# Kernel tuning notes

Measured on AMD Instinct MI355X. Metric: run time of the kernel, lower is better.

The kernel has to match this reference:

```python
import jax, jax.numpy as jnp
import numpy as np

B, S, C, H, D = 4, 2048, 512, 8, 64
EPS = 1e-5
SCALE = D ** -0.5


def layer_norm(x, w, b):
    m = jnp.mean(x, axis=-1, keepdims=True)
    v = jnp.var(x, axis=-1, keepdims=True)
    return (x - m) * jax.lax.rsqrt(v + EPS) * w + b


def setup_inputs() -> dict:
    key = jax.random.key(0)
    ks = jax.random.split(key, 7)
    s = 0.02
    return {
        "x": jax.random.normal(ks[0], (B, S, C), jnp.float32),
        "Wq": jax.random.normal(ks[1], (C, H * D), jnp.float32) * s,
        "Wk": jax.random.normal(ks[2], (C, H * D), jnp.float32) * s,
        "Wv": jax.random.normal(ks[3], (C, H * D), jnp.float32) * s,
        "Wo": jax.random.normal(ks[4], (H * D, C), jnp.float32) * s,
        "ln1_w": jnp.ones((C,), jnp.float32), "ln1_b": jnp.zeros((C,), jnp.float32),
        "ff_ln1_w": jnp.ones((C,), jnp.float32), "ff_ln1_b": jnp.zeros((C,), jnp.float32),
        "ff_w1": jax.random.normal(ks[5], (C, C), jnp.float32) * s, "ff_b1": jnp.zeros((C,), jnp.float32),
        "ff_ln2_w": jnp.ones((C,), jnp.float32), "ff_ln2_b": jnp.zeros((C,), jnp.float32),
        "ff_w2": jax.random.normal(ks[6], (C, C), jnp.float32) * s, "ff_b2": jnp.zeros((C,), jnp.float32),
        "ln2_w": jnp.ones((C,), jnp.float32), "ln2_b": jnp.zeros((C,), jnp.float32),
    }


def causal_attention(x, Wq, Wk, Wv, Wo):
    # Mathematically identical to the bucketed memory-efficient attention:
    # online-softmax bucketing changes compute order, not the result.
    q = (x @ Wq).reshape(B, S, H, D).transpose(0, 2, 1, 3)  # [B,H,S,D]
    k = (x @ Wk).reshape(B, S, H, D).transpose(0, 2, 1, 3)
    v = (x @ Wv).reshape(B, S, H, D).transpose(0, 2, 1, 3)
    scores = jnp.einsum('bhqd,bhkd->bhqk', q, k) * SCALE  # [B,H,S,S]
    causal = jnp.tril(jnp.ones((S, S), bool))
    scores = jnp.where(causal, scores, jnp.finfo(scores.dtype).min)
    attn = jax.nn.softmax(scores, axis=-1)
    out = jnp.einsum('bhqk,bhkd->bhqd', attn, v)
    out = out.transpose(0, 2, 1, 3).reshape(B, S, H * D)
    return out @ Wo


def reference(x, Wq, Wk, Wv, Wo, ln1_w, ln1_b, ff_ln1_w, ff_ln1_b, ff_w1, ff_b1,
              ff_ln2_w, ff_ln2_b, ff_w2, ff_b2, ln2_w, ln2_b):
    a = causal_attention(x, Wq, Wk, Wv, Wo)
    x_ln = layer_norm(a + x, ln1_w, ln1_b)
    h = layer_norm(x_ln, ff_ln1_w, ff_ln1_b) @ ff_w1 + ff_b1
    h = layer_norm(h, ff_ln2_w, ff_ln2_b) @ ff_w2 + ff_b2
    return layer_norm(h + x_ln, ln2_w, ln2_b)
```

## Files before the change

### kernel.cpp

```cpp
#include <hip/hip_runtime.h>

#define B_ 4
#define S_ 2048
#define C_ 512
#define H_ 8
#define D_ 64
#define M_ 8192

typedef short s8v __attribute__((ext_vector_type(8)));
typedef short s4v __attribute__((ext_vector_type(4)));
typedef float f4v __attribute__((ext_vector_type(4)));
typedef unsigned short u16;
typedef unsigned int u32;

__device__ __forceinline__ u16 f2b(float f) {
    u32 u = __builtin_bit_cast(u32, f);
    u = u + 0x7fffu + ((u >> 16) & 1u);
    return (u16)(u >> 16);
}

__device__ __forceinline__ void b2f8(const s8v v, float* f) {
    #pragma unroll
    for (int k = 0; k < 8; ++k)
        f[k] = __builtin_bit_cast(float, (u32)(u16)v[k] << 16);
}

__device__ __forceinline__ void gl2lds16(const void* g, void* l) {
    __builtin_amdgcn_global_load_lds(
        (const __attribute__((address_space(1))) void*)g,
        (__attribute__((address_space(3))) void*)l, 16, 0, 0);
}

__global__ __launch_bounds__(256) void prep_k(const float* __restrict__ x,
                                              u16* __restrict__ xb,
                                              const float* __restrict__ s0,
                                              const float* __restrict__ s1,
                                              const float* __restrict__ s2,
                                              const float* __restrict__ s3,
                                              const float* __restrict__ s4,
                                              const float* __restrict__ s5,
                                              u16* __restrict__ d0,
                                              u16* __restrict__ d1,
                                              u16* __restrict__ d2,
                                              u16* __restrict__ d3,
                                              u16* __restrict__ d4,
                                              u16* __restrict__ d5)
{
    __shared__ float t[32][33];
    const int bx = blockIdx.x;
    if (bx < 4096) {
        const int i = (bx * 256 + (int)threadIdx.x) * 4;
        const float4 v = *(const float4*)&x[i];
        ushort4 o;
        o.x = f2b(v.x); o.y = f2b(v.y); o.z = f2b(v.z); o.w = f2b(v.w);
        *(ushort4*)&xb[i] = o;
        return;
    }
    const int tb = bx - 4096;
    const int z = tb >> 8, rem = tb & 255;
    const float* W; u16* Wt;
    switch (z) {
        case 0: W = s0; Wt = d0; break;
        case 1: W = s1; Wt = d1; break;
        case 2: W = s2; Wt = d2; break;
        case 3: W = s3; Wt = d3; break;
        case 4: W = s4; Wt = d4; break;
        default: W = s5; Wt = d5; break;
    }
    const int tx = threadIdx.x & 31, ty = threadIdx.x >> 5;
    const int n0 = (rem & 15) * 32, k0 = (rem >> 4) * 32;
    #pragma unroll
    for (int i = 0; i < 4; ++i)
        t[ty + i * 8][tx] = W[(size_t)(k0 + ty + i * 8) * C_ + n0 + tx];
    __syncthreads();
    #pragma unroll
    for (int i = 0; i < 4; ++i)
        Wt[(size_t)(n0 + ty + i * 8) * C_ + k0 + tx] = f2b(t[tx][ty + i * 8]);
}

template <bool OB>
__global__ __launch_bounds__(256) void gemm_k(const u16* __restrict__ A,
                                              const u16* __restrict__ Bt,
                                              const float* __restrict__ bias,
                                              void* __restrict__ outv)
{
    __shared__ u16 As[2][128][64];
    __shared__ u16 Bs[2][64][64];
    const int tid = threadIdx.x;
    const int lane = tid & 63, w = tid >> 6;
    const int q4 = lane >> 4, l16 = lane & 15;
    const int wr = w >> 1, wc = w & 1;
    const int bm = blockIdx.x * 128, bn = blockIdx.y * 64;
    const int sr8  = lane >> 3;
    const int scol = ((lane & 7) ^ sr8) * 8;

    f4v acc[4][2];
    #pragma unroll
    for (int i = 0; i < 4; ++i)
        #pragma unroll
        for (int j = 0; j < 2; ++j) acc[i][j] = (f4v){0.f, 0.f, 0.f, 0.f};

    const u16* Ab = A  + (size_t)bm * C_;
    const u16* Bb = Bt + (size_t)bn * C_;

    auto stage = [&](int bf, int kt) {
        const int k0 = kt * 64;
        #pragma unroll
        for (int t = 0; t < 4; ++t)
            gl2lds16(Ab + (size_t)(w * 32 + t * 8 + sr8) * C_ + k0 + scol,
                     (char*)As + bf * 16384 + (w * 32 + t * 8) * 128);
        #pragma unroll
        for (int t = 0; t < 2; ++t)
            gl2lds16(Bb + (size_t)(w * 16 + t * 8 + sr8) * C_ + k0 + scol,
                     (char*)Bs + bf * 8192 + (w * 16 + t * 8) * 128);
    };

    stage(0, 0);
    for (int kt = 0; kt < 8; ++kt) {
        __syncthreads();
        const int bf = kt & 1;
        if (kt < 7) stage(bf ^ 1, kt + 1);
        #pragma unroll
        for (int kk = 0; kk < 2; ++kk) {
            const int pc = ((kk * 4 + q4) ^ (l16 & 7)) * 8;
            s8v a[4], b[2];
            #pragma unroll
            for (int i = 0; i < 4; ++i)
                a[i] = *(const s8v*)&As[bf][wr * 64 + i * 16 + l16][pc];
            #pragma unroll
            for (int j = 0; j < 2; ++j)
                b[j] = *(const s8v*)&Bs[bf][wc * 32 + j * 16 + l16][pc];
            #pragma unroll
            for (int i = 0; i < 4; ++i)
                #pragma unroll
                for (int j = 0; j < 2; ++j)
                    acc[i][j] = __builtin_amdgcn_mfma_f32_16x16x32_bf16(a[i], b[j], acc[i][j], 0, 0, 0);
        }
    }

    if constexpr (OB) {
        __syncthreads();
        u16* Ls = (u16*)As;
        #pragma unroll
        for (int j = 0; j < 2; ++j) {
            const int nl = wc * 32 + j * 16 + l16;
            const float bj = bias ? bias[bn + nl] : 0.0f;
            #pragma unroll
            for (int i = 0; i < 4; ++i) {
                const int ml = wr * 64 + i * 16 + q4 * 4;
                #pragma unroll
                for (int reg = 0; reg < 4; ++reg)
                    Ls[(ml + reg) * 72 + nl] = f2b(acc[i][j][reg] + bj);
            }
        }
        __syncthreads();
        #pragma unroll
        for (int pass = 0; pass < 4; ++pass) {
            const int idx = tid + pass * 256;
            const int r = idx >> 3, c = idx & 7;
            const s8v v = *(const s8v*)&Ls[r * 72 + c * 8];
            *(s8v*)&((u16*)outv)[(size_t)(bm + r) * C_ + bn + c * 8] = v;
        }
    } else {
        #pragma unroll
        for (int j = 0; j < 2; ++j) {
            const int n = bn + wc * 32 + j * 16 + l16;
            const float bj = bias ? bias[n] : 0.0f;
            #pragma unroll
            for (int i = 0; i < 4; ++i) {
                const int m = bm + wr * 64 + i * 16 + q4 * 4;
                #pragma unroll
                for (int reg = 0; reg < 4; ++reg)
                    ((float*)outv)[(size_t)(m + reg) * C_ + n] = acc[i][j][reg] + bj;
            }
        }
    }
}

__global__ __launch_bounds__(256) void qkv_k(const u16* __restrict__ A,
                                             const u16* __restrict__ Wq,
                                             const u16* __restrict__ Wk,
                                             const u16* __restrict__ Wv,
                                             u16* __restrict__ oq,
                                             u16* __restrict__ ok,
                                             u16* __restrict__ ovt)
{
    __shared__ u16 As[2][128][64];
    __shared__ u16 Bs[2][64][64];
    const int tid = threadIdx.x;
    const int lane = tid & 63, w = tid >> 6;
    const int q4 = lane >> 4, l16 = lane & 15;
    const int wr = w >> 1, wc = w & 1;
    const int nt = blockIdx.y, which = nt >> 3;
    const u16* Bt = which == 0 ? Wq : (which == 1 ? Wk : Wv);
    const int bm = blockIdx.x * 128, bn = (nt & 7) * 64;
    const int sr8  = lane >> 3;
    const int scol = ((lane & 7) ^ sr8) * 8;

    f4v acc[4][2];
    #pragma unroll
    for (int i = 0; i < 4; ++i)
        #pragma unroll
        for (int j = 0; j < 2; ++j) acc[i][j] = (f4v){0.f, 0.f, 0.f, 0.f};

    const u16* Ab = A  + (size_t)bm * C_;
    const u16* Bb = Bt + (size_t)bn * C_;

    auto stage = [&](int bf, int kt) {
        const int k0 = kt * 64;
        #pragma unroll
        for (int t = 0; t < 4; ++t)
            gl2lds16(Ab + (size_t)(w * 32 + t * 8 + sr8) * C_ + k0 + scol,
                     (char*)As + bf * 16384 + (w * 32 + t * 8) * 128);
        #pragma unroll
        for (int t = 0; t < 2; ++t)
            gl2lds16(Bb + (size_t)(w * 16 + t * 8 + sr8) * C_ + k0 + scol,
                     (char*)Bs + bf * 8192 + (w * 16 + t * 8) * 128);
    };

    stage(0, 0);
    for (int kt = 0; kt < 8; ++kt) {
        __syncthreads();
        const int bf = kt & 1;
        if (kt < 7) stage(bf ^ 1, kt + 1);
        #pragma unroll
        for (int kk = 0; kk < 2; ++kk) {
            const int pc = ((kk * 4 + q4) ^ (l16 & 7)) * 8;
            s8v a[4], b[2];
            #pragma unroll
            for (int i = 0; i < 4; ++i)
                a[i] = *(const s8v*)&As[bf][wr * 64 + i * 16 + l16][pc];
            #pragma unroll
            for (int j = 0; j < 2; ++j)
                b[j] = *(const s8v*)&Bs[bf][wc * 32 + j * 16 + l16][pc];
            #pragma unroll
            for (int i = 0; i < 4; ++i)
                #pragma unroll
                for (int j = 0; j < 2; ++j)
                    acc[i][j] = __builtin_amdgcn_mfma_f32_16x16x32_bf16(a[i], b[j], acc[i][j], 0, 0, 0);
        }
    }

    if (which < 2) {
        __syncthreads();
        u16* Ls = (u16*)As;
        #pragma unroll
        for (int j = 0; j < 2; ++j) {
            const int nl = wc * 32 + j * 16 + l16;
            #pragma unroll
            for (int i = 0; i < 4; ++i) {
                const int ml = wr * 64 + i * 16 + q4 * 4;
                #pragma unroll
                for (int reg = 0; reg < 4; ++reg)
                    Ls[(ml + reg) * 72 + nl] = f2b(acc[i][j][reg]);
            }
        }
        __syncthreads();
        u16* dst = which == 0 ? oq : ok;
        #pragma unroll
        for (int pass = 0; pass < 4; ++pass) {
            const int idx = tid + pass * 256;
            const int r = idx >> 3, c = idx & 7;
            const s8v v = *(const s8v*)&Ls[r * 72 + c * 8];
            const int cg = which == 0 ? c : ((c & ~3) | ((c & 3) ^ ((r >> 2) & 3)));
            *(s8v*)&dst[(size_t)(bm + r) * C_ + bn + cg * 8] = v;
        }
    } else {
        const int bglob = bm >> 11;
        const int sbase = bm & (S_ - 1);
        #pragma unroll
        for (int j = 0; j < 2; ++j) {
            const int n = bn + wc * 32 + j * 16 + l16;
            const int h = n >> 6, d = n & 63;
            u16* vrow = ovt + ((size_t)(bglob * H_ + h) * D_ + d) * S_;
            const int xw = d & 7;
            #pragma unroll
            for (int i = 0; i < 4; ++i) {
                const int s = sbase + wr * 64 + i * 16 + q4 * 4;
                const int pg = ((s & 31) >> 2) ^ xw;
                s4v pv;
                #pragma unroll
                for (int reg = 0; reg < 4; ++reg) pv[reg] = (short)f2b(acc[i][j][reg]);
                *(s4v*)&vrow[(s & ~31) + (pg << 2)] = pv;
            }
        }
    }
}

__global__ __launch_bounds__(256) void ln2xb_k(const u16* __restrict__ in,
                                               const float* __restrict__ res,
                                               const float* __restrict__ w1,
                                               const float* __restrict__ b1,
                                               const float* __restrict__ w2,
                                               const float* __restrict__ b2,
                                               u16* __restrict__ out1,
                                               u16* __restrict__ out2)
{
    const int lane = threadIdx.x & 63;
    const int row  = blockIdx.x * 4 + (threadIdx.x >> 6);
    const size_t off = (size_t)row * C_ + lane * 8;
    float v[8];
    b2f8(*(const s8v*)&in[off], v);
    {
        const float4 r0 = *(const float4*)&res[off];
        const float4 r1 = *(const float4*)&res[off + 4];
        v[0] += r0.x; v[1] += r0.y; v[2] += r0.z; v[3] += r0.w;
        v[4] += r1.x; v[5] += r1.y; v[6] += r1.z; v[7] += r1.w;
    }
    float s = 0.f, ss = 0.f;
    #pragma unroll
    for (int k = 0; k < 8; ++k) { s += v[k]; ss += v[k] * v[k]; }
    #pragma unroll
    for (int o = 32; o >= 1; o >>= 1) { s += __shfl_xor(s, o); ss += __shfl_xor(ss, o); }
    float mean = s * (1.0f / C_);
    float rstd = rsqrtf(ss * (1.0f / C_) - mean * mean + 1e-5f);

    const float4 wA0 = *(const float4*)&w1[lane * 8];
    const float4 wA1 = *(const float4*)&w1[lane * 8 + 4];
    const float4 bA0 = *(const float4*)&b1[lane * 8];
    const float4 bA1 = *(const float4*)&b1[lane * 8 + 4];
    const float wA[8] = {wA0.x, wA0.y, wA0.z, wA0.w, wA1.x, wA1.y, wA1.z, wA1.w};
    const float bA[8] = {bA0.x, bA0.y, bA0.z, bA0.w, bA1.x, bA1.y, bA1.z, bA1.w};
    float y[8];
    s8v o1;
    #pragma unroll
    for (int k = 0; k < 8; ++k) {
        y[k] = (v[k] - mean) * rstd * wA[k] + bA[k];
        o1[k] = (short)f2b(y[k]);
    }
    *(s8v*)&out1[off] = o1;

    s = 0.f; ss = 0.f;
    #pragma unroll
    for (int k = 0; k < 8; ++k) { s += y[k]; ss += y[k] * y[k]; }
    #pragma unroll
    for (int o = 32; o >= 1; o >>= 1) { s += __shfl_xor(s, o); ss += __shfl_xor(ss, o); }
    mean = s * (1.0f / C_);
    rstd = rsqrtf(ss * (1.0f / C_) - mean * mean + 1e-5f);

    const float4 wB0 = *(const float4*)&w2[lane * 8];
    const float4 wB1 = *(const float4*)&w2[lane * 8 + 4];
    const float4 bB0 = *(const float4*)&b2[lane * 8];
    const float4 bB1 = *(const float4*)&b2[lane * 8 + 4];
    const float wB[8] = {wB0.x, wB0.y, wB0.z, wB0.w, wB1.x, wB1.y, wB1.z, wB1.w};
    const float bB[8] = {bB0.x, bB0.y, bB0.z, bB0.w, bB1.x, bB1.y, bB1.z, bB1.w};
    s8v o2;
    #pragma unroll
    for (int k = 0; k < 8; ++k)
        o2[k] = (short)f2b((y[k] - mean) * rstd * wB[k] + bB[k]);
    *(s8v*)&out2[off] = o2;
}

__global__ __launch_bounds__(256) void lnb_k(const u16* __restrict__ in,
                                             const float* __restrict__ w,
                                             const float* __restrict__ bb,
                                             u16* __restrict__ out)
{
    const int lane = threadIdx.x & 63;
    const int row  = blockIdx.x * 4 + (threadIdx.x >> 6);
    const size_t off = (size_t)row * C_ + lane * 8;
    float v[8];
    b2f8(*(const s8v*)&in[off], v);
    float s = 0.f, ss = 0.f;
    #pragma unroll
    for (int k = 0; k < 8; ++k) { s += v[k]; ss += v[k] * v[k]; }
    #pragma unroll
    for (int o = 32; o >= 1; o >>= 1) { s += __shfl_xor(s, o); ss += __shfl_xor(ss, o); }
    const float mean = s * (1.0f / C_);
    const float rstd = rsqrtf(ss * (1.0f / C_) - mean * mean + 1e-5f);
    const float4 w0 = *(const float4*)&w[lane * 8];
    const float4 w1 = *(const float4*)&w[lane * 8 + 4];
    const float4 b0 = *(const float4*)&bb[lane * 8];
    const float4 b1 = *(const float4*)&bb[lane * 8 + 4];
    const float wv[8] = {w0.x, w0.y, w0.z, w0.w, w1.x, w1.y, w1.z, w1.w};
    const float bv[8] = {b0.x, b0.y, b0.z, b0.w, b1.x, b1.y, b1.z, b1.w};
    s8v o;
    #pragma unroll
    for (int k = 0; k < 8; ++k)
        o[k] = (short)f2b((v[k] - mean) * rstd * wv[k] + bv[k]);
    *(s8v*)&out[off] = o;
}

__global__ __launch_bounds__(256) void lnfin_k(const u16* __restrict__ in,
                                               const u16* __restrict__ res,
                                               const float* __restrict__ w,
                                               const float* __restrict__ bb,
                                               float* __restrict__ out)
{
    const int lane = threadIdx.x & 63;
    const int row  = blockIdx.x * 4 + (threadIdx.x >> 6);
    const size_t off = (size_t)row * C_ + lane * 8;
    float v[8], r[8];
    b2f8(*(const s8v*)&in[off], v);
    b2f8(*(const s8v*)&res[off], r);
    #pragma unroll
    for (int k = 0; k < 8; ++k) v[k] += r[k];
    float s = 0.f, ss = 0.f;
    #pragma unroll
    for (int k = 0; k < 8; ++k) { s += v[k]; ss += v[k] * v[k]; }
    #pragma unroll
    for (int o = 32; o >= 1; o >>= 1) { s += __shfl_xor(s, o); ss += __shfl_xor(ss, o); }
    const float mean = s * (1.0f / C_);
    const float rstd = rsqrtf(ss * (1.0f / C_) - mean * mean + 1e-5f);
    const float4 w0 = *(const float4*)&w[lane * 8];
    const float4 w1 = *(const float4*)&w[lane * 8 + 4];
    const float4 b0 = *(const float4*)&bb[lane * 8];
    const float4 b1 = *(const float4*)&bb[lane * 8 + 4];
    const float wv[8] = {w0.x, w0.y, w0.z, w0.w, w1.x, w1.y, w1.z, w1.w};
    const float bv[8] = {b0.x, b0.y, b0.z, b0.w, b1.x, b1.y, b1.z, b1.w};
    float4 o0, o1;
    o0.x = (v[0] - mean) * rstd * wv[0] + bv[0];
    o0.y = (v[1] - mean) * rstd * wv[1] + bv[1];
    o0.z = (v[2] - mean) * rstd * wv[2] + bv[2];
    o0.w = (v[3] - mean) * rstd * wv[3] + bv[3];
    o1.x = (v[4] - mean) * rstd * wv[4] + bv[4];
    o1.y = (v[5] - mean) * rstd * wv[5] + bv[5];
    o1.z = (v[6] - mean) * rstd * wv[6] + bv[6];
    o1.w = (v[7] - mean) * rstd * wv[7] + bv[7];
    *(float4*)&out[off]     = o0;
    *(float4*)&out[off + 4] = o1;
}

__global__ __launch_bounds__(512, 4) void attn_k(const u16* __restrict__ Q,
                                                 const u16* __restrict__ K,
                                                 const u16* __restrict__ Vt,
                                                 u16* __restrict__ O)
{
    __shared__ char smem[65536];
    u16* KsB = (u16*)smem;
    u16* VsB = (u16*)(smem + 32768);
    const int tid = threadIdx.x;
    const int lane = tid & 63, w = tid >> 6;
    const int grp = w >> 2, wl = w & 3;
    const int q4 = lane >> 4, l16 = lane & 15;
    const int h = blockIdx.x, px = blockIdx.y, b = blockIdx.z;
    const int qH = 31 - px, qL = px;
    const int nH = 32 - px;
    const size_t base  = ((size_t)b * S_) * C_ + h * D_;
    const size_t basev = ((size_t)(b * H_ + h)) * D_ * S_;
    const int lr = lane >> 2, lc = (lane & 3) * 8;
    const int kq = (q4 ^ ((l16 >> 2) & 3)) * 8;
    const int qrow = wl * 16 + l16;

    const u16* ksA = KsB + grp * 4096;
    const u16* ksBp = KsB + (grp + 2) * 4096;
    const u16* vsA = VsB + grp * 4096;
    const u16* vsBp = VsB + (grp + 2) * 4096;
    char* kdA = (char*)KsB + grp * 8192 + wl * 1024;
    char* kdB = (char*)KsB + (grp + 2) * 8192 + wl * 1024;
    char* vdA = (char*)VsB + grp * 8192 + wl * 1024;
    char* vdB = (char*)VsB + (grp + 2) * 8192 + wl * 1024;

    const int kfb = l16 * 32 + kq;
    int vfb[4];
    #pragma unroll
    for (int c = 0; c < 4; ++c)
        vfb[c] = l16 * 32 + ((((c & 1) * 4 + q4) ^ (l16 & 7)) * 4);

    const u16* kpt = K  + base  + (size_t)(wl * 16 + lr) * C_ + lc;
    const u16* vpt = Vt + basev + (size_t)(wl * 16 + lr) * S_ + lc;

    f4v acc[4]; float lp[4];
    f4v oH[4];  float lpH[4];
    #pragma unroll
    for (int j = 0; j < 4; ++j) {
        acc[j] = (f4v){0.f, 0.f, 0.f, 0.f}; lp[j] = 0.f;
        oH[j]  = (f4v){0.f, 0.f, 0.f, 0.f}; lpH[j] = 0.f;
    }
    s8v qf[2];
    #pragma unroll
    for (int kh = 0; kh < 2; ++kh)
        qf[kh] = *(const s8v*)&Q[base + (size_t)(qH * 64 + qrow) * C_ + kh * 32 + q4 * 8];

    bool dumped = false, wrapped = false;

    auto dumpacc = [&]() {
        #pragma unroll
        for (int j = 0; j < 4; ++j) {
            oH[j] = acc[j]; lpH[j] = lp[j];
            acc[j] = (f4v){0.f, 0.f, 0.f, 0.f}; lp[j] = 0.f;
        }
        #pragma unroll
        for (int kh = 0; kh < 2; ++kh)
            qf[kh] = *(const s8v*)&Q[base + (size_t)(qL * 64 + qrow) * C_ + kh * 32 + q4 * 8];
    };

    auto compute = [&](const u16* ks, const u16* vs, const bool diag) {
        f4v sc[4];
        #pragma unroll
        for (int j = 0; j < 4; ++j) sc[j] = (f4v){0.f, 0.f, 0.f, 0.f};
        __builtin_amdgcn_s_setprio(1);
        #pragma unroll
        for (int kh = 0; kh < 2; ++kh)
            #pragma unroll
            for (int j = 0; j < 4; ++j) {
                const s8v kf = *(const s8v*)&ks[kfb + kh * 2048 + j * 512];
                sc[j] = __builtin_amdgcn_mfma_f32_16x16x32_bf16(kf, qf[kh], sc[j], 0, 0, 0);
            }
        __builtin_amdgcn_s_setprio(0);
        s4v pa[4];
        if (diag) {
            #pragma unroll
            for (int j = 0; j < 4; ++j) {
                float ps = 0.0f;
                #pragma unroll
                for (int reg = 0; reg < 4; ++reg) {
                    float tt = fmaf(sc[j][reg], 0.18033688011112043f, -11.541560327111707f);
                    if ((j * 16 + q4 * 4 + reg) > qrow) tt = -128.0f;
                    const float p = exp2f(tt);
                    ps += p;
                    pa[j][reg] = (short)(__builtin_bit_cast(u32, p) >> 16);
                }
                lp[j] += ps;
            }
        } else {
            #pragma unroll
            for (int j = 0; j < 4; ++j) {
                float ps = 0.0f;
                #pragma unroll
                for (int reg = 0; reg < 4; ++reg) {
                    const float p = exp2f(fmaf(sc[j][reg], 0.18033688011112043f,
                                               -11.541560327111707f));
                    ps += p;
                    pa[j][reg] = (short)(__builtin_bit_cast(u32, p) >> 16);
                }
                lp[j] += ps;
            }
        }
        __builtin_amdgcn_s_setprio(1);
        #pragma unroll
        for (int c = 0; c < 4; ++c)
            #pragma unroll
            for (int dj = 0; dj < 4; ++dj) {
                const s4v vb = *(const s4v*)&vs[vfb[c] + (c >> 1) * 2048 + dj * 512];
                acc[dj] = __builtin_amdgcn_mfma_f32_16x16x16bf16_1k(pa[c], vb, acc[dj], 0, 0, 0);
            }
        __builtin_amdgcn_s_setprio(0);
    };

    {
        const u16* kc = kpt + (size_t)(grp * 64) * C_;
        const u16* vc = vpt + grp * 64;
        gl2lds16(kc, kdA); gl2lds16(kc + 32, kdA + 4096);
        gl2lds16(vc, vdA); gl2lds16(vc + 32, vdA + 4096);
    }
    const u16* kcur = kpt + (size_t)((grp + 2) * 64) * C_;
    const u16* vcur = vpt + (grp + 2) * 64;
    int snext = grp + 2;
    int s = grp;

    auto advance = [&]() {
        kcur += (size_t)128 * C_;
        vcur += 128;
        snext += 2;
        if (!wrapped && snext >= nH) {
            kcur -= (size_t)(nH * 64) * C_;
            vcur -= nH * 64;
            wrapped = true;
        }
    };

    for (int u = 0; u < 8; ++u) {
        __syncthreads();
        {
            gl2lds16(kcur, kdB); gl2lds16(kcur + 32, kdB + 4096);
            gl2lds16(vcur, vdB); gl2lds16(vcur + 32, vdB + 4096);
            advance();
        }
        if (!dumped && s >= nH) { dumped = true; dumpacc(); }
        compute(ksA, vsA, (s == nH - 1) || (s == 32));
        s += 2;
        __syncthreads();
        if (u < 7 || grp == 0) {
            gl2lds16(kcur, kdA); gl2lds16(kcur + 32, kdA + 4096);
            gl2lds16(vcur, vdA); gl2lds16(vcur + 32, vdA + 4096);
            advance();
        }
        if (!dumped && s >= nH) { dumped = true; dumpacc(); }
        compute(ksBp, vsBp, (s == nH - 1) || (s == 32));
        s += 2;
    }
    __syncthreads();
    if (grp == 0) {
        if (!dumped) { dumped = true; dumpacc(); }
        compute(ksA, vsA, true);
    }
    if (!dumped) {
        #pragma unroll
        for (int j = 0; j < 4; ++j) {
            oH[j] = acc[j]; lpH[j] = lp[j];
            acc[j] = (f4v){0.f, 0.f, 0.f, 0.f}; lp[j] = 0.f;
        }
    }

    __syncthreads();
    float* exH = (float*)smem;
    float* exL = (float*)(smem + 20480);
    {
        float* p = (grp ? exH : exL) + (wl * 64 + lane) * 20;
        if (grp) {
            #pragma unroll
            for (int dj = 0; dj < 4; ++dj)
                #pragma unroll
                for (int reg = 0; reg < 4; ++reg) p[dj * 4 + reg] = oH[dj][reg];
            #pragma unroll
            for (int j = 0; j < 4; ++j) p[16 + j] = lpH[j];
        } else {
            #pragma unroll
            for (int dj = 0; dj < 4; ++dj)
                #pragma unroll
                for (int reg = 0; reg < 4; ++reg) p[dj * 4 + reg] = acc[dj][reg];
            #pragma unroll
            for (int j = 0; j < 4; ++j) p[16 + j] = lp[j];
        }
    }
    __syncthreads();
    if (grp == 0) {
        const float* p = exH + (wl * 64 + lane) * 20;
        #pragma unroll
        for (int dj = 0; dj < 4; ++dj)
            #pragma unroll
            for (int reg = 0; reg < 4; ++reg) oH[dj][reg] += p[dj * 4 + reg];
        #pragma unroll
        for (int j = 0; j < 4; ++j) lpH[j] += p[16 + j];
        float lt = (lpH[0] + lpH[1]) + (lpH[2] + lpH[3]);
        lt += __shfl_xor(lt, 16);
        lt += __shfl_xor(lt, 32);
        #pragma unroll
        for (int reg = 0; reg < 4; ++reg) {
            const float inv = 1.0f / __shfl(lt, q4 * 4 + reg);
            const size_t rowoff = base + (size_t)(qH * 64 + wl * 16 + q4 * 4 + reg) * C_;
            #pragma unroll
            for (int dj = 0; dj < 4; ++dj)
                O[rowoff + dj * 16 + l16] = f2b(oH[dj][reg] * inv);
        }
    } else {
        const float* p = exL + (wl * 64 + lane) * 20;
        #pragma unroll
        for (int dj = 0; dj < 4; ++dj)
            #pragma unroll
            for (int reg = 0; reg < 4; ++reg) acc[dj][reg] += p[dj * 4 + reg];
        #pragma unroll
        for (int j = 0; j < 4; ++j) lp[j] += p[16 + j];
        float lt = (lp[0] + lp[1]) + (lp[2] + lp[3]);
        lt += __shfl_xor(lt, 16);
        lt += __shfl_xor(lt, 32);
        #pragma unroll
        for (int reg = 0; reg < 4; ++reg) {
            const float inv = 1.0f / __shfl(lt, q4 * 4 + reg);
            const size_t rowoff = base + (size_t)(qL * 64 + wl * 16 + q4 * 4 + reg) * C_;
            #pragma unroll
            for (int dj = 0; dj < 4; ++dj)
                O[rowoff + dj * 16 + l16] = f2b(acc[dj][reg] * inv);
        }
    }
}

extern "C" void kernel_launch(void* const* d_in, const int* in_sizes, int n_in,
                              void* d_out, int out_size, void* d_ws, size_t ws_size,
                              hipStream_t stream)
{
    const float* x       = (const float*)d_in[0];
    const float* Wq      = (const float*)d_in[1];
    const float* Wk      = (const float*)d_in[2];
    const float* Wv      = (const float*)d_in[3];
    const float* Wo      = (const float*)d_in[4];
    const float* ln1_w   = (const float*)d_in[5];
    const float* ln1_b   = (const float*)d_in[6];
    const float* ffln1_w = (const float*)d_in[7];
    const float* ffln1_b = (const float*)d_in[8];
    const float* ff_w1   = (const float*)d_in[9];
    const float* ff_b1   = (const float*)d_in[10];
    const float* ffln2_w = (const float*)d_in[11];
    const float* ffln2_b = (const float*)d_in[12];
    const float* ff_w2   = (const float*)d_in[13];
    const float* ff_b2   = (const float*)d_in[14];
    const float* ln2_w   = (const float*)d_in[15];
    const float* ln2_b   = (const float*)d_in[16];
    float* out = (float*)d_out;

    const size_t MC = (size_t)M_ * C_;
    const size_t WW = (size_t)C_ * C_;
    u16* xb   = (u16*)d_ws;
    u16* WqT  = xb + MC;
    u16* WkT  = WqT + WW;
    u16* WvT  = WkT + WW;
    u16* WoT  = WvT + WW;
    u16* W1T  = WoT + WW;
    u16* W2T  = W1T + WW;
    u16* qbuf = W2T + WW;
    u16* kbuf = qbuf + MC;
    u16* vbuf = kbuf + MC;
    u16* vtbuf= vbuf + MC;
    u16*  abuf = xb;
    u16*  tf   = qbuf;
    u16*  xln  = vbuf;

    const dim3 gg(M_ / 128, C_ / 64);
    const dim3 gq(M_ / 128, 24);
    const dim3 ga(H_, 16, B_);
    const int  gl = M_ / 4;

    prep_k<<<5632, 256, 0, stream>>>(x, xb, Wq, Wk, Wv, Wo, ff_w1, ff_w2,
                                     WqT, WkT, WvT, WoT, W1T, W2T);

    qkv_k<<<gq, 256, 0, stream>>>(xb, WqT, WkT, WvT, qbuf, kbuf, vtbuf);
    attn_k<<<ga, 512, 0, stream>>>(qbuf, kbuf, vtbuf, abuf);

    gemm_k<true><<<gg, 256, 0, stream>>>(abuf, WoT, nullptr, tf);
    ln2xb_k<<<gl, 256, 0, stream>>>(tf, x, ln1_w, ln1_b, ffln1_w, ffln1_b,
                                    xln, xb);
    gemm_k<true><<<gg, 256, 0, stream>>>(xb, W1T, ff_b1, tf);
    lnb_k<<<gl, 256, 0, stream>>>(tf, ffln2_w, ffln2_b, xb);
    gemm_k<true><<<gg, 256, 0, stream>>>(xb, W2T, ff_b2, tf);
    lnfin_k<<<gl, 256, 0, stream>>>(tf, xln, ln2_w, ln2_b, out);
}
```

Measured before the change: 219.7 us.

## Halve attention key tile to 32 and double blocks per CU

The causal attention kernel now streams K/V in 32-key sub-tiles instead of 64-key tiles. That halves the shared-memory staging buffers and each compute step's score and probability registers, and the occupancy hint rises from 4 to 8 blocks. Loop count, wrap logic, diagonal masking (now with a per-subtile offset) and the final tail step are reworked to match. The goal is higher occupancy and better latency hiding, at the cost of twice as many barriers and smaller MFMA batches per sync.

```diff
diff --git a/kernel.cpp b/kernel.cpp
--- a/kernel.cpp
+++ b/kernel.cpp
@@ -421,52 +421,53 @@
     *(float4*)&out[off + 4] = o1;
 }
 
-__global__ __launch_bounds__(512, 4) void attn_k(const u16* __restrict__ Q,
+__global__ __launch_bounds__(512, 8) void attn_k(const u16* __restrict__ Q,
                                                  const u16* __restrict__ K,
                                                  const u16* __restrict__ Vt,
                                                  u16* __restrict__ O)
 {
-    __shared__ char smem[65536];
+    __shared__ char smem[40960];
     u16* KsB = (u16*)smem;
-    u16* VsB = (u16*)(smem + 32768);
+    u16* VsB = (u16*)(smem + 16384);
     const int tid = threadIdx.x;
     const int lane = tid & 63, w = tid >> 6;
     const int grp = w >> 2, wl = w & 3;
     const int q4 = lane >> 4, l16 = lane & 15;
     const int h = blockIdx.x, px = blockIdx.y, b = blockIdx.z;
     const int qH = 31 - px, qL = px;
-    const int nH = 32 - px;
+    const int nHp = 64 - 2 * px;
     const size_t base  = ((size_t)b * S_) * C_ + h * D_;
     const size_t basev = ((size_t)(b * H_ + h)) * D_ * S_;
-    const int lr = lane >> 2, lc = (lane & 3) * 8;
     const int kq = (q4 ^ ((l16 >> 2) & 3)) * 8;
     const int qrow = wl * 16 + l16;
 
-    const u16* ksA = KsB + grp * 4096;
-    const u16* ksBp = KsB + (grp + 2) * 4096;
-    const u16* vsA = VsB + grp * 4096;
-    const u16* vsBp = VsB + (grp + 2) * 4096;
-    char* kdA = (char*)KsB + grp * 8192 + wl * 1024;
-    char* kdB = (char*)KsB + (grp + 2) * 8192 + wl * 1024;
-    char* vdA = (char*)VsB + grp * 8192 + wl * 1024;
-    char* vdB = (char*)VsB + (grp + 2) * 8192 + wl * 1024;
+    const u16* ksA  = KsB + grp * 2048;
+    const u16* ksBp = KsB + (grp + 2) * 2048;
+    const u16* vsA  = VsB + grp * 2048;
+    const u16* vsBp = VsB + (grp + 2) * 2048;
+    char* kdA = (char*)KsB + grp * 4096 + wl * 1024;
+    char* kdB = (char*)KsB + (grp + 2) * 4096 + wl * 1024;
+    char* vdA = (char*)VsB + grp * 4096 + wl * 1024;
+    char* vdB = (char*)VsB + (grp + 2) * 4096 + wl * 1024;
 
     const int kfb = l16 * 32 + kq;
-    int vfb[4];
-    #pragma unroll
-    for (int c = 0; c < 4; ++c)
-        vfb[c] = l16 * 32 + ((((c & 1) * 4 + q4) ^ (l16 & 7)) * 4);
-
-    const u16* kpt = K  + base  + (size_t)(wl * 16 + lr) * C_ + lc;
-    const u16* vpt = Vt + basev + (size_t)(wl * 16 + lr) * S_ + lc;
-
-    f4v acc[4]; float lp[4];
-    f4v oH[4];  float lpH[4];
+    int vfb[2];
+    #pragma unroll
+    for (int c = 0; c < 2; ++c)
+        vfb[c] = l16 * 32 + ((((c * 4 + q4)) ^ (l16 & 7)) * 4);
+
+    const int ldr = wl * 16 + (lane >> 2);
+    const u16* kpt2 = K  + base  + (size_t)(ldr & 31) * C_ + (ldr >> 5) * 32 + (lane & 3) * 8;
+    const u16* vpt2 = Vt + basev + (size_t)ldr * S_ + (lane & 3) * 8;
+
+    f4v acc[4]; float lp[2];
+    f4v oH[4];  float lpH[2];
     #pragma unroll
     for (int j = 0; j < 4; ++j) {
-        acc[j] = (f4v){0.f, 0.f, 0.f, 0.f}; lp[j] = 0.f;
-        oH[j]  = (f4v){0.f, 0.f, 0.f, 0.f}; lpH[j] = 0.f;
-    }
+        acc[j] = (f4v){0.f, 0.f, 0.f, 0.f};
+        oH[j]  = (f4v){0.f, 0.f, 0.f, 0.f};
+    }
+    lp[0] = lp[1] = lpH[0] = lpH[1] = 0.f;
     s8v qf[2];
     #pragma unroll
     for (int kh = 0; kh < 2; ++kh)
@@ -477,36 +478,37 @@
     auto dumpacc = [&]() {
         #pragma unroll
         for (int j = 0; j < 4; ++j) {
-            oH[j] = acc[j]; lpH[j] = lp[j];
-            acc[j] = (f4v){0.f, 0.f, 0.f, 0.f}; lp[j] = 0.f;
-        }
+            oH[j] = acc[j];
+            acc[j] = (f4v){0.f, 0.f, 0.f, 0.f};
+        }
+        lpH[0] = lp[0]; lpH[1] = lp[1]; lp[0] = lp[1] = 0.f;
         #pragma unroll
         for (int kh = 0; kh < 2; ++kh)
             qf[kh] = *(const s8v*)&Q[base + (size_t)(qL * 64 + qrow) * C_ + kh * 32 + q4 * 8];
     };
 
-    auto compute = [&](const u16* ks, const u16* vs, const bool diag) {
-        f4v sc[4];
-        #pragma unroll
-        for (int j = 0; j < 4; ++j) sc[j] = (f4v){0.f, 0.f, 0.f, 0.f};
+    auto compute = [&](const u16* ks, const u16* vs, const int mbase) {
+        f4v sc[2];
+        sc[0] = (f4v){0.f, 0.f, 0.f, 0.f};
+        sc[1] = (f4v){0.f, 0.f, 0.f, 0.f};
         __builtin_amdgcn_s_setprio(1);
         #pragma unroll
         for (int kh = 0; kh < 2; ++kh)
             #pragma unroll
-            for (int j = 0; j < 4; ++j) {
-                const s8v kf = *(const s8v*)&ks[kfb + kh * 2048 + j * 512];
+            for (int j = 0; j < 2; ++j) {
+                const s8v kf = *(const s8v*)&ks[kfb + kh * 1024 + j * 512];
                 sc[j] = __builtin_amdgcn_mfma_f32_16x16x32_bf16(kf, qf[kh], sc[j], 0, 0, 0);
             }
         __builtin_amdgcn_s_setprio(0);
-        s4v pa[4];
-        if (diag) {
-            #pragma unroll
-            for (int j = 0; j < 4; ++j) {
+        s4v pa[2];
+        if (mbase >= 0) {
+            #pragma unroll
+            for (int j = 0; j < 2; ++j) {
                 float ps = 0.0f;
                 #pragma unroll
                 for (int reg = 0; reg < 4; ++reg) {
                     float tt = fmaf(sc[j][reg], 0.18033688011112043f, -11.541560327111707f);
-                    if ((j * 16 + q4 * 4 + reg) > qrow) tt = -128.0f;
+                    if ((mbase + j * 16 + q4 * 4 + reg) > qrow) tt = -128.0f;
                     const float p = exp2f(tt);
                     ps += p;
                     pa[j][reg] = (short)(__builtin_bit_cast(u32, p) >> 16);
@@ -515,7 +517,7 @@
             }
         } else {
             #pragma unroll
-            for (int j = 0; j < 4; ++j) {
+            for (int j = 0; j < 2; ++j) {
                 float ps = 0.0f;
                 #pragma unroll
                 for (int reg = 0; reg < 4; ++reg) {
@@ -529,69 +531,54 @@
         }
         __builtin_amdgcn_s_setprio(1);
         #pragma unroll
-        for (int c = 0; c < 4; ++c)
+        for (int c = 0; c < 2; ++c)
             #pragma unroll
             for (int dj = 0; dj < 4; ++dj) {
-                const s4v vb = *(const s4v*)&vs[vfb[c] + (c >> 1) * 2048 + dj * 512];
+                const s4v vb = *(const s4v*)&vs[vfb[c] + dj * 512];
                 acc[dj] = __builtin_amdgcn_mfma_f32_16x16x16bf16_1k(pa[c], vb, acc[dj], 0, 0, 0);
             }
         __builtin_amdgcn_s_setprio(0);
     };
 
-    {
-        const u16* kc = kpt + (size_t)(grp * 64) * C_;
-        const u16* vc = vpt + grp * 64;
-        gl2lds16(kc, kdA); gl2lds16(kc + 32, kdA + 4096);
-        gl2lds16(vc, vdA); gl2lds16(vc + 32, vdA + 4096);
-    }
-    const u16* kcur = kpt + (size_t)((grp + 2) * 64) * C_;
-    const u16* vcur = vpt + (grp + 2) * 64;
+    gl2lds16(kpt2 + (size_t)(grp * 32) * C_, kdA);
+    gl2lds16(vpt2 + grp * 32, vdA);
+    const u16* kcur = kpt2 + (size_t)((grp + 2) * 32) * C_;
+    const u16* vcur = vpt2 + (grp + 2) * 32;
     int snext = grp + 2;
     int s = grp;
 
     auto advance = [&]() {
-        kcur += (size_t)128 * C_;
-        vcur += 128;
+        kcur += (size_t)64 * C_;
+        vcur += 64;
         snext += 2;
-        if (!wrapped && snext >= nH) {
-            kcur -= (size_t)(nH * 64) * C_;
-            vcur -= nH * 64;
+        if (!wrapped && snext >= nHp) {
+            kcur -= (size_t)(nHp * 32) * C_;
+            vcur -= nHp * 32;
             wrapped = true;
         }
     };
 
-    for (int u = 0; u < 8; ++u) {
+    for (int u = 0; u < 16; ++u) {
         __syncthreads();
+        gl2lds16(kcur, kdB); gl2lds16(vcur, vdB); advance();
+        if (!dumped && s >= nHp) { dumped = true; dumpacc(); }
         {
-            gl2lds16(kcur, kdB); gl2lds16(kcur + 32, kdB + 4096);
-            gl2lds16(vcur, vdB); gl2lds16(vcur + 32, vdB + 4096);
-            advance();
-        }
-        if (!dumped && s >= nH) { dumped = true; dumpacc(); }
-        compute(ksA, vsA, (s == nH - 1) || (s == 32));
+            const int mb = (s >= nHp - 2 && s < nHp) ? (s - (nHp - 2)) * 32 : -1;
+            compute(ksA, vsA, mb);
+        }
         s += 2;
         __syncthreads();
-        if (u < 7 || grp == 0) {
-            gl2lds16(kcur, kdA); gl2lds16(kcur + 32, kdA + 4096);
-            gl2lds16(vcur, vdA); gl2lds16(vcur + 32, vdA + 4096);
-            advance();
-        }
-        if (!dumped && s >= nH) { dumped = true; dumpacc(); }
-        compute(ksBp, vsBp, (s == nH - 1) || (s == 32));
+        gl2lds16(kcur, kdA); gl2lds16(vcur, vdA); advance();
+        if (!dumped && s >= nHp) { dumped = true; dumpacc(); }
+        {
+            const int mb = (s >= nHp - 2 && s < nHp) ? (s - (nHp - 2)) * 32 : -1;
+            compute(ksBp, vsBp, mb);
+        }
         s += 2;
     }
     __syncthreads();
-    if (grp == 0) {
-        if (!dumped) { dumped = true; dumpacc(); }
-        compute(ksA, vsA, true);
-    }
-    if (!dumped) {
-        #pragma unroll
-        for (int j = 0; j < 4; ++j) {
-            oH[j] = acc[j]; lpH[j] = lp[j];
-            acc[j] = (f4v){0.f, 0.f, 0.f, 0.f}; lp[j] = 0.f;
-        }
-    }
+    if (!dumped) { dumped = true; dumpacc(); }
+    compute(ksA, vsA, (s - 64) * 32);
 
     __syncthreads();
     float* exH = (float*)smem;
@@ -603,15 +590,13 @@
             for (int dj = 0; dj < 4; ++dj)
                 #pragma unroll
                 for (int reg = 0; reg < 4; ++reg) p[dj * 4 + reg] = oH[dj][reg];
-            #pragma unroll
-            for (int j = 0; j < 4; ++j) p[16 + j] = lpH[j];
+            p[16] = lpH[0]; p[17] = lpH[1];
         } else {
             #pragma unroll
             for (int dj = 0; dj < 4; ++dj)
                 #pragma unroll
                 for (int reg = 0; reg < 4; ++reg) p[dj * 4 + reg] = acc[dj][reg];
-            #pragma unroll
-            for (int j = 0; j < 4; ++j) p[16 + j] = lp[j];
+            p[16] = lp[0]; p[17] = lp[1];
         }
     }
     __syncthreads();
@@ -621,9 +606,8 @@
         for (int dj = 0; dj < 4; ++dj)
             #pragma unroll
             for (int reg = 0; reg < 4; ++reg) oH[dj][reg] += p[dj * 4 + reg];
-        #pragma unroll
-        for (int j = 0; j < 4; ++j) lpH[j] += p[16 + j];
-        float lt = (lpH[0] + lpH[1]) + (lpH[2] + lpH[3]);
+        lpH[0] += p[16]; lpH[1] += p[17];
+        float lt = lpH[0] + lpH[1];
         lt += __shfl_xor(lt, 16);
         lt += __shfl_xor(lt, 32);
         #pragma unroll
@@ -640,9 +624,8 @@
         for (int dj = 0; dj < 4; ++dj)
             #pragma unroll
             for (int reg = 0; reg < 4; ++reg) acc[dj][reg] += p[dj * 4 + reg];
-        #pragma unroll
-        for (int j = 0; j < 4; ++j) lp[j] += p[16 + j];
-        float lt = (lp[0] + lp[1]) + (lp[2] + lp[3]);
+        lp[0] += p[16]; lp[1] += p[17];
+        float lt = lp[0] + lp[1];
         lt += __shfl_xor(lt, 16);
         lt += __shfl_xor(lt, 32);
         #pragma unroll
```

Result: slower. 244.6 us (+11.3%).

## Split GEMM K-dimension across two wave groups with LDS reduction

Applied to the files above, without the earlier changes.

The projection GEMM kernel now launches 512 threads, and two groups of four waves each handle half of the K range (256 each) with their own double-buffered LDS tiles. At the end, group 1 writes its partial accumulators to LDS and group 0 adds them before the bias/bf16 epilogue. This is intended to raise parallelism and latency hiding for the small-K (512) GEMMs with only 512 blocks. The cost is extra LDS traffic, extra barriers for the reduction, and lower per-block occupancy.

```diff
diff --git a/kernel.cpp b/kernel.cpp
--- a/kernel.cpp
+++ b/kernel.cpp
@@ -79,20 +79,23 @@
 }
 
 template <bool OB>
-__global__ __launch_bounds__(256) void gemm_k(const u16* __restrict__ A,
+__global__ __launch_bounds__(512) void gemm_k(const u16* __restrict__ A,
                                               const u16* __restrict__ Bt,
                                               const float* __restrict__ bias,
                                               void* __restrict__ outv)
 {
-    __shared__ u16 As[2][128][64];
-    __shared__ u16 Bs[2][64][64];
+    __shared__ char smem[49152];
+    u16* As2 = (u16*)smem;
+    u16* Bs2 = (u16*)(smem + 32768);
     const int tid = threadIdx.x;
     const int lane = tid & 63, w = tid >> 6;
+    const int grp = w >> 2, wl = w & 3;
     const int q4 = lane >> 4, l16 = lane & 15;
-    const int wr = w >> 1, wc = w & 1;
+    const int wr = wl >> 1, wc = wl & 1;
     const int bm = blockIdx.x * 128, bn = blockIdx.y * 64;
-    const int sr8  = lane >> 3;
-    const int scol = ((lane & 7) ^ sr8) * 8;
+    const int sr   = lane >> 2;
+    const int scol = ((lane & 3) ^ ((lane >> 3) & 3)) * 8;
+    const int pc   = (q4 ^ ((l16 >> 1) & 3)) * 8;
 
     f4v acc[4][2];
     #pragma unroll
@@ -100,78 +103,102 @@
         #pragma unroll
         for (int j = 0; j < 2; ++j) acc[i][j] = (f4v){0.f, 0.f, 0.f, 0.f};
 
-    const u16* Ab = A  + (size_t)bm * C_;
-    const u16* Bb = Bt + (size_t)bn * C_;
-
-    auto stage = [&](int bf, int kt) {
-        const int k0 = kt * 64;
-        #pragma unroll
-        for (int t = 0; t < 4; ++t)
-            gl2lds16(Ab + (size_t)(w * 32 + t * 8 + sr8) * C_ + k0 + scol,
-                     (char*)As + bf * 16384 + (w * 32 + t * 8) * 128);
-        #pragma unroll
-        for (int t = 0; t < 2; ++t)
-            gl2lds16(Bb + (size_t)(w * 16 + t * 8 + sr8) * C_ + k0 + scol,
-                     (char*)Bs + bf * 8192 + (w * 16 + t * 8) * 128);
+    const u16* Ab = A  + (size_t)bm * C_ + grp * 256;
+    const u16* Bb = Bt + (size_t)bn * C_ + grp * 256;
+    char* adst = (char*)As2 + grp * 16384;
+    char* bdst = (char*)Bs2 + grp * 8192;
+
+    auto stage = [&](int bf, int t) {
+        const int k0 = t * 32;
+        #pragma unroll
+        for (int r = 0; r < 2; ++r)
+            gl2lds16(Ab + (size_t)((r * 4 + wl) * 16 + sr) * C_ + k0 + scol,
+                     adst + bf * 8192 + (r * 4 + wl) * 1024);
+        gl2lds16(Bb + (size_t)(wl * 16 + sr) * C_ + k0 + scol,
+                 bdst + bf * 4096 + wl * 1024);
     };
 
     stage(0, 0);
-    for (int kt = 0; kt < 8; ++kt) {
+    for (int t = 0; t < 8; ++t) {
         __syncthreads();
-        const int bf = kt & 1;
-        if (kt < 7) stage(bf ^ 1, kt + 1);
-        #pragma unroll
-        for (int kk = 0; kk < 2; ++kk) {
-            const int pc = ((kk * 4 + q4) ^ (l16 & 7)) * 8;
-            s8v a[4], b[2];
+        const int bf = t & 1;
+        if (t < 7) stage(bf ^ 1, t + 1);
+        const u16* Ar = As2 + grp * 8192 + bf * 4096;
+        const u16* Br = Bs2 + grp * 4096 + bf * 2048;
+        s8v a[4], b[2];
+        #pragma unroll
+        for (int i = 0; i < 4; ++i)
+            a[i] = *(const s8v*)&Ar[(wr * 64 + i * 16 + l16) * 32 + pc];
+        #pragma unroll
+        for (int j = 0; j < 2; ++j)
+            b[j] = *(const s8v*)&Br[(wc * 32 + j * 16 + l16) * 32 + pc];
+        #pragma unroll
+        for (int i = 0; i < 4; ++i)
+            #pragma unroll
+            for (int j = 0; j < 2; ++j)
+                acc[i][j] = __builtin_amdgcn_mfma_f32_16x16x32_bf16(a[i], b[j], acc[i][j], 0, 0, 0);
+    }
+
+    __syncthreads();
+    float* ex = (float*)smem;
+    if (grp == 1) {
+        #pragma unroll
+        for (int j = 0; j < 2; ++j)
             #pragma unroll
             for (int i = 0; i < 4; ++i)
-                a[i] = *(const s8v*)&As[bf][wr * 64 + i * 16 + l16][pc];
-            #pragma unroll
-            for (int j = 0; j < 2; ++j)
-                b[j] = *(const s8v*)&Bs[bf][wc * 32 + j * 16 + l16][pc];
+                #pragma unroll
+                for (int reg = 0; reg < 4; ++reg)
+                    ex[(wr * 64 + i * 16 + q4 * 4 + reg) * 64 + wc * 32 + j * 16 + l16] = acc[i][j][reg];
+    }
+    __syncthreads();
+    if (grp == 0) {
+        #pragma unroll
+        for (int j = 0; j < 2; ++j)
             #pragma unroll
             for (int i = 0; i < 4; ++i)
                 #pragma unroll
-                for (int j = 0; j < 2; ++j)
-                    acc[i][j] = __builtin_amdgcn_mfma_f32_16x16x32_bf16(a[i], b[j], acc[i][j], 0, 0, 0);
-        }
-    }
+                for (int reg = 0; reg < 4; ++reg)
+                    acc[i][j][reg] += ex[(wr * 64 + i * 16 + q4 * 4 + reg) * 64 + wc * 32 + j * 16 + l16];
+    }
+    __syncthreads();
 
     if constexpr (OB) {
+        u16* Ls = (u16*)smem;
+        if (grp == 0) {
+            #pragma unroll
+            for (int j = 0; j < 2; ++j) {
+                const int nl = wc * 32 + j * 16 + l16;
+                const float bj = bias ? bias[bn + nl] : 0.0f;
+                #pragma unroll
+                for (int i = 0; i < 4; ++i) {
+                    const int ml = wr * 64 + i * 16 + q4 * 4;
+                    #pragma unroll
+                    for (int reg = 0; reg < 4; ++reg)
+                        Ls[(ml + reg) * 72 + nl] = f2b(acc[i][j][reg] + bj);
+                }
+            }
+        }
         __syncthreads();
-        u16* Ls = (u16*)As;
-        #pragma unroll
-        for (int j = 0; j < 2; ++j) {
-            const int nl = wc * 32 + j * 16 + l16;
-            const float bj = bias ? bias[bn + nl] : 0.0f;
-            #pragma unroll
-            for (int i = 0; i < 4; ++i) {
-                const int ml = wr * 64 + i * 16 + q4 * 4;
-                #pragma unroll
-                for (int reg = 0; reg < 4; ++reg)
-                    Ls[(ml + reg) * 72 + nl] = f2b(acc[i][j][reg] + bj);
-            }
-        }
-        __syncthreads();
-        #pragma unroll
-        for (int pass = 0; pass < 4; ++pass) {
-            const int idx = tid + pass * 256;
+        #pragma unroll
+        for (int pass = 0; pass < 2; ++pass) {
+            const int idx = tid + pass * 512;
             const int r = idx >> 3, c = idx & 7;
             const s8v v = *(const s8v*)&Ls[r * 72 + c * 8];
             *(s8v*)&((u16*)outv)[(size_t)(bm + r) * C_ + bn + c * 8] = v;
         }
     } else {
-        #pragma unroll
-        for (int j = 0; j < 2; ++j) {
-            const int n = bn + wc * 32 + j * 16 + l16;
-            const float bj = bias ? bias[n] : 0.0f;
-            #pragma unroll
-            for (int i = 0; i < 4; ++i) {
-                const int m = bm + wr * 64 + i * 16 + q4 * 4;
-                #pragma unroll
-                for (int reg = 0; reg < 4; ++reg)
-                    ((float*)outv)[(size_t)(m + reg) * C_ + n] = acc[i][j][reg] + bj;
+        if (grp == 0) {
+            #pragma unroll
+            for (int j = 0; j < 2; ++j) {
+                const int n = bn + wc * 32 + j * 16 + l16;
+                const float bj = bias ? bias[n] : 0.0f;
+                #pragma unroll
+                for (int i = 0; i < 4; ++i) {
+                    const int m = bm + wr * 64 + i * 16 + q4 * 4;
+                    #pragma unroll
+                    for (int reg = 0; reg < 4; ++reg)
+                        ((float*)outv)[(size_t)(m + reg) * C_ + n] = acc[i][j][reg] + bj;
+                }
             }
         }
     }
@@ -438,7 +465,6 @@
     const int nH = 32 - px;
     const size_t base  = ((size_t)b * S_) * C_ + h * D_;
     const size_t basev = ((size_t)(b * H_ + h)) * D_ * S_;
-    const int lr = lane >> 2, lc = (lane & 3) * 8;
     const int kq = (q4 ^ ((l16 >> 2) & 3)) * 8;
     const int qrow = wl * 16 + l16;
 
@@ -457,8 +483,8 @@
     for (int c = 0; c < 4; ++c)
         vfb[c] = l16 * 32 + ((((c & 1) * 4 + q4) ^ (l16 & 7)) * 4);
 
-    const u16* kpt = K  + base  + (size_t)(wl * 16 + lr) * C_ + lc;
-    const u16* vpt = Vt + basev + (size_t)(wl * 16 + lr) * S_ + lc;
+    const u16* kpt = K  + base  + (size_t)(wl * 16 + (lane >> 2)) * C_ + (lane & 3) * 8;
+    const u16* vpt = Vt + basev + (size_t)(wl * 16 + (lane >> 2)) * S_ + (lane & 3) * 8;
 
     f4v acc[4]; float lp[4];
     f4v oH[4];  float lpH[4];
@@ -707,11 +733,11 @@
     qkv_k<<<gq, 256, 0, stream>>>(xb, WqT, WkT, WvT, qbuf, kbuf, vtbuf);
     attn_k<<<ga, 512, 0, stream>>>(qbuf, kbuf, vtbuf, abuf);
 
-    gemm_k<true><<<gg, 256, 0, stream>>>(abuf, WoT, nullptr, tf);
+    gemm_k<true><<<gg, 512, 0, stream>>>(abuf, WoT, nullptr, tf);
     ln2xb_k<<<gl, 256, 0, stream>>>(tf, x, ln1_w, ln1_b, ffln1_w, ffln1_b,
                                     xln, xb);
-    gemm_k<true><<<gg, 256, 0, stream>>>(xb, W1T, ff_b1, tf);
+    gemm_k<true><<<gg, 512, 0, stream>>>(xb, W1T, ff_b1, tf);
     lnb_k<<<gl, 256, 0, stream>>>(tf, ffln2_w, ffln2_b, xb);
-    gemm_k<true><<<gg, 256, 0, stream>>>(xb, W2T, ff_b2, tf);
+    gemm_k<true><<<gg, 512, 0, stream>>>(xb, W2T, ff_b2, tf);
     lnfin_k<<<gl, 256, 0, stream>>>(tf, xln, ln2_w, ln2_b, out);
 }
```

Result: no change. 220.3 us (+0.3%).
